# Optimization experiments

Hardware: AMD Instinct MI355X
Metric: run time of the kernel (lower is better)

Reference implementation:

```python
import jax, jax.numpy as jnp
import numpy as np

LAMB_LABELS = 1.0
LAMB_BBOXES = 5.0
LAMB_GENIOU = 2.0


def box_cxcywh_to_xyxy(x):
    cx, cy, w, h = x[..., 0], x[..., 1], x[..., 2], x[..., 3]
    return jnp.stack([cx - 0.5 * w, cy - 0.5 * h, cx + 0.5 * w, cy + 0.5 * h], axis=-1)


def generalized_box_iou(b1, b2):
    # b1: [P,4] xyxy, b2: [T,4] xyxy -> [P,T] pairwise GIoU
    area1 = (b1[:, 2] - b1[:, 0]) * (b1[:, 3] - b1[:, 1])
    area2 = (b2[:, 2] - b2[:, 0]) * (b2[:, 3] - b2[:, 1])
    lt = jnp.maximum(b1[:, None, :2], b2[None, :, :2])
    rb = jnp.minimum(b1[:, None, 2:], b2[None, :, 2:])
    wh = jnp.clip(rb - lt, 0.0)
    inter = wh[..., 0] * wh[..., 1]
    union = area1[:, None] + area2[None, :] - inter
    iou = inter / union
    lt_e = jnp.minimum(b1[:, None, :2], b2[None, :, :2])
    rb_e = jnp.maximum(b1[:, None, 2:], b2[None, :, 2:])
    wh_e = jnp.clip(rb_e - lt_e, 0.0)
    area_e = wh_e[..., 0] * wh_e[..., 1]
    return iou - (area_e - union) / area_e


def setup_inputs() -> dict:
    key = jax.random.key(0)
    k1, k2, k3, k4 = jax.random.split(key, 4)
    B, N, C, T = 16, 900, 92, 960
    out_labels = jax.random.normal(k1, (B, N, C), dtype=jnp.float32)
    out_bboxes = jax.random.uniform(k2, (B, N, 4), dtype=jnp.float32)
    tgt_labels = jax.random.randint(k3, (T,), 0, C, dtype=jnp.int64)
    tgt_bboxes = jax.random.uniform(k4, (T, 4), dtype=jnp.float32)
    return {"out_labels": out_labels, "out_bboxes": out_bboxes,
            "tgt_labels": tgt_labels, "tgt_bboxes": tgt_bboxes}


def reference(out_labels, out_bboxes, tgt_labels, tgt_bboxes):
    B, N, C = out_labels.shape
    # '(b n) d' softmax over classes, then gather target-label columns
    probs = jax.nn.softmax(out_labels.reshape(B * N, C), axis=-1)
    cost_labels = 1.0 - probs[:, tgt_labels]                     # [BN, T]
    ob = out_bboxes.reshape(B * N, 4)
    # pairwise L1 (torch.cdist p=1)
    cost_bboxes = jnp.sum(jnp.abs(ob[:, None, :] - tgt_bboxes[None, :, :]), axis=-1)
    # NOTE: original converts only predicted boxes to xyxy (targets used as-is)
    cost_geniou = 1.0 - generalized_box_iou(box_cxcywh_to_xyxy(ob), tgt_bboxes)
    cost = (LAMB_LABELS * cost_labels + LAMB_BBOXES * cost_bboxes
            + LAMB_GENIOU * cost_geniou)
    return cost.reshape(B, N, -1)                                # [B, N, T]
```

## Files before the change

kernel.cpp:

```cpp
#include <hip/hip_runtime.h>
#include <math.h>

constexpr int kC = 92, kT = 960;
constexpr int kBN = 14400;
constexpr int WPB = 8;
constexpr int THREADS = WPB * 64;

__global__ __launch_bounds__(THREADS, 6) void matcher_kernel(
    const float* __restrict__ out_labels,
    const float* __restrict__ out_bboxes,
    const int*   __restrict__ tgt_labels,
    const float* __restrict__ tgt_bboxes,
    float*       __restrict__ cost)
{
    __shared__ float s_cls[WPB][96];

    const int tid  = threadIdx.x;
    const int w    = tid >> 6;
    const int lane = tid & 63;
    const int p    = blockIdx.x * WPB + w;

    const float* lrow = out_labels + (size_t)p * kC;
    float e0 = __expf(lrow[lane]);
    float e1 = (lane + 64 < kC) ? __expf(lrow[lane + 64]) : 0.0f;
    float s = e0 + e1;
    #pragma unroll
    for (int m = 1; m < 64; m <<= 1)
        s += __shfl_xor(s, m, 64);
    float inv = __builtin_amdgcn_rcpf(s);
    s_cls[w][lane] = fmaf(-e0, inv, 5.0f);
    if (lane + 64 < kC) s_cls[w][lane + 64] = fmaf(-e1, inv, 5.0f);

    float4 bb = ((const float4*)out_bboxes)[p];
    float hw = 0.5f * bb.z, hh = 0.5f * bb.w;
    float bx0 = bb.x - hw, by0 = bb.y - hh;
    float bx1 = bb.x + hw, by1 = bb.y + hh;
    float area1 = (bx1 - bx0) * (by1 - by0);

    asm volatile("s_waitcnt lgkmcnt(0)" ::: "memory");

    const float4* tb4 = (const float4*)tgt_bboxes;
    float* crow = cost + (size_t)p * kT;
    #pragma unroll 5
    for (int k = 0; k < 15; ++k) {
        const int t = lane + 64 * k;
        float4 tbb = tb4[t];
        int    lb  = tgt_labels[t];
        float  cls = s_cls[w][lb];
        float  a2  = (tbb.z - tbb.x) * (tbb.w - tbb.y);
        float l1 = fabsf(bb.x - tbb.x) + fabsf(bb.y - tbb.y)
                 + fabsf(bb.z - tbb.z) + fabsf(bb.w - tbb.w);
        float ltx = fmaxf(bx0, tbb.x), lty = fmaxf(by0, tbb.y);
        float rbx = fminf(bx1, tbb.z), rby = fminf(by1, tbb.w);
        float iw = fmaxf(rbx - ltx, 0.0f), ih = fmaxf(rby - lty, 0.0f);
        float inter = iw * ih;
        float uni = area1 + a2 - inter;
        float ex0 = fminf(bx0, tbb.x), ey0 = fminf(by0, tbb.y);
        float ex1 = fmaxf(bx1, tbb.z), ey1 = fmaxf(by1, tbb.w);
        float area_e = (ex1 - ex0) * (ey1 - ey0);
        float num = fmaf(uni, uni, inter * area_e);
        float rcp = __builtin_amdgcn_rcpf(uni * area_e);
        float v = fmaf(5.0f, l1, cls);
        v = fmaf(-2.0f * num, rcp, v);
        crow[t] = v;
    }
}

extern "C" void kernel_launch(void* const* d_in, const int* in_sizes, int n_in,
                              void* d_out, int out_size, void* d_ws, size_t ws_size,
                              hipStream_t stream) {
    const float* out_labels = (const float*)d_in[0];
    const float* out_bboxes = (const float*)d_in[1];
    const int*   tgt_labels = (const int*)d_in[2];
    const float* tgt_bboxes = (const float*)d_in[3];
    float* cost = (float*)d_out;
    dim3 grid(kBN / WPB);
    matcher_kernel<<<grid, THREADS, 0, stream>>>(out_labels, out_bboxes,
                                                 tgt_labels, tgt_bboxes, cost);
}
```

Before: 90.29 us.

## Process two prediction rows per wavefront and use packed float2 math

After: 88.65 us. No clear change (-1.8%).

```diff
diff --git a/kernel.cpp b/kernel.cpp
--- a/kernel.cpp
+++ b/kernel.cpp
@@ -3,66 +3,89 @@
 
 constexpr int kC = 92, kT = 960;
 constexpr int kBN = 14400;
-constexpr int WPB = 8;
+constexpr int WPB = 4;
 constexpr int THREADS = WPB * 64;
 
-__global__ __launch_bounds__(THREADS, 6) void matcher_kernel(
+typedef float vf2 __attribute__((ext_vector_type(2)));
+
+__global__ __launch_bounds__(THREADS, 8) void matcher_kernel(
     const float* __restrict__ out_labels,
     const float* __restrict__ out_bboxes,
     const int*   __restrict__ tgt_labels,
     const float* __restrict__ tgt_bboxes,
     float*       __restrict__ cost)
 {
-    __shared__ float s_cls[WPB][96];
+    __shared__ float2 s_cl2[WPB][96];
 
     const int tid  = threadIdx.x;
     const int w    = tid >> 6;
     const int lane = tid & 63;
-    const int p    = blockIdx.x * WPB + w;
+    const int p0   = (blockIdx.x * WPB + w) * 2;
 
-    const float* lrow = out_labels + (size_t)p * kC;
-    float e0 = __expf(lrow[lane]);
-    float e1 = (lane + 64 < kC) ? __expf(lrow[lane + 64]) : 0.0f;
-    float s = e0 + e1;
+    const float* lr0 = out_labels + (size_t)p0 * kC;
+    const float* lr1 = lr0 + kC;
+    float e00 = __expf(lr0[lane]);
+    float e10 = __expf(lr1[lane]);
+    float e01 = (lane + 64 < kC) ? __expf(lr0[lane + 64]) : 0.0f;
+    float e11 = (lane + 64 < kC) ? __expf(lr1[lane + 64]) : 0.0f;
+    float s0 = e00 + e01, s1 = e10 + e11;
     #pragma unroll
-    for (int m = 1; m < 64; m <<= 1)
-        s += __shfl_xor(s, m, 64);
-    float inv = __builtin_amdgcn_rcpf(s);
-    s_cls[w][lane] = fmaf(-e0, inv, 5.0f);
-    if (lane + 64 < kC) s_cls[w][lane + 64] = fmaf(-e1, inv, 5.0f);
+    for (int m = 1; m < 64; m <<= 1) {
+        s0 += __shfl_xor(s0, m, 64);
+        s1 += __shfl_xor(s1, m, 64);
+    }
+    float inv0 = __builtin_amdgcn_rcpf(s0);
+    float inv1 = __builtin_amdgcn_rcpf(s1);
+    s_cl2[w][lane] = make_float2(fmaf(-e00, inv0, 5.0f), fmaf(-e10, inv1, 5.0f));
+    if (lane + 64 < kC)
+        s_cl2[w][lane + 64] =
+            make_float2(fmaf(-e01, inv0, 5.0f), fmaf(-e11, inv1, 5.0f));
 
-    float4 bb = ((const float4*)out_bboxes)[p];
-    float hw = 0.5f * bb.z, hh = 0.5f * bb.w;
-    float bx0 = bb.x - hw, by0 = bb.y - hh;
-    float bx1 = bb.x + hw, by1 = bb.y + hh;
-    float area1 = (bx1 - bx0) * (by1 - by0);
+    float4 bbA = ((const float4*)out_bboxes)[p0];
+    float4 bbB = ((const float4*)out_bboxes)[p0 + 1];
+    vf2 bcA = {bbA.x, bbA.y}, whA = {bbA.z, bbA.w};
+    vf2 bcB = {bbB.x, bbB.y}, whB = {bbB.z, bbB.w};
+    vf2 hA = whA * 0.5f,  hB = whB * 0.5f;
+    vf2 b0A = bcA - hA,   b1A = bcA + hA;
+    vf2 b0B = bcB - hB,   b1B = bcB + hB;
+    float area1A = (b1A.x - b0A.x) * (b1A.y - b0A.y);
+    float area1B = (b1B.x - b0B.x) * (b1B.y - b0B.y);
 
     asm volatile("s_waitcnt lgkmcnt(0)" ::: "memory");
 
     const float4* tb4 = (const float4*)tgt_bboxes;
-    float* crow = cost + (size_t)p * kT;
+    float* crow0 = cost + (size_t)p0 * kT;
+    float* crow1 = crow0 + kT;
+
+    auto row_cost = [&](vf2 b0, vf2 b1, vf2 bc, vf2 wh, float area1,
+                        vf2 t0, vf2 t1, vf2 wt, float a2, float cls) -> float {
+        vf2 lt = {fmaxf(b0.x, t0.x), fmaxf(b0.y, t0.y)};
+        vf2 rb = {fminf(b1.x, t1.x), fminf(b1.y, t1.y)};
+        vf2 iwu = rb - lt;
+        float iw = fmaxf(iwu.x, 0.0f), ih = fmaxf(iwu.y, 0.0f);
+        float inter = iw * ih;
+        vf2 ew = (wh + wt) - iwu;
+        float area_e = ew.x * ew.y;
+        float uni = (area1 + a2) - inter;
+        vf2 d0 = bc - t0, d1 = wh - t1;
+        float l1 = fabsf(d0.x) + fabsf(d0.y) + fabsf(d1.x) + fabsf(d1.y);
+        float num = fmaf(uni, uni, inter * area_e);
+        float rcp = __builtin_amdgcn_rcpf(uni * area_e);
+        float v = fmaf(5.0f, l1, cls);
+        return fmaf(-2.0f * num, rcp, v);
+    };
+
     #pragma unroll 5
     for (int k = 0; k < 15; ++k) {
         const int t = lane + 64 * k;
         float4 tbb = tb4[t];
         int    lb  = tgt_labels[t];
-        float  cls = s_cls[w][lb];
-        float  a2  = (tbb.z - tbb.x) * (tbb.w - tbb.y);
-        float l1 = fabsf(bb.x - tbb.x) + fabsf(bb.y - tbb.y)
-                 + fabsf(bb.z - tbb.z) + fabsf(bb.w - tbb.w);
-        float ltx = fmaxf(bx0, tbb.x), lty = fmaxf(by0, tbb.y);
-        float rbx = fminf(bx1, tbb.z), rby = fminf(by1, tbb.w);
-        float iw = fmaxf(rbx - ltx, 0.0f), ih = fmaxf(rby - lty, 0.0f);
-        float inter = iw * ih;
-        float uni = area1 + a2 - inter;
-        float ex0 = fminf(bx0, tbb.x), ey0 = fminf(by0, tbb.y);
-        float ex1 = fmaxf(bx1, tbb.z), ey1 = fmaxf(by1, tbb.w);
-        float area_e = (ex1 - ex0) * (ey1 - ey0);
-        float num = fmaf(uni, uni, inter * area_e);
-        float rcp = __builtin_amdgcn_rcpf(uni * area_e);
-        float v = fmaf(5.0f, l1, cls);
-        v = fmaf(-2.0f * num, rcp, v);
-        crow[t] = v;
+        float2 cls = s_cl2[w][lb];
+        vf2 t0 = {tbb.x, tbb.y}, t1 = {tbb.z, tbb.w};
+        vf2 wt = t1 - t0;
+        float a2 = wt.x * wt.y;
+        crow0[t] = row_cost(b0A, b1A, bcA, whA, area1A, t0, t1, wt, a2, cls.x);
+        crow1[t] = row_cost(b0B, b1B, bcB, whB, area1B, t0, t1, wt, a2, cls.y);
     }
 }
 
@@ -74,7 +97,7 @@
     const int*   tgt_labels = (const int*)d_in[2];
     const float* tgt_bboxes = (const float*)d_in[3];
     float* cost = (float*)d_out;
-    dim3 grid(kBN / WPB);
+    dim3 grid(kBN / (WPB * 2));
     matcher_kernel<<<grid, THREADS, 0, stream>>>(out_labels, out_bboxes,
                                                  tgt_labels, tgt_bboxes, cost);
 }
```
